# Kernel tuning notes

Measured on AMD Instinct MI355X. Metric: run time of the kernel, lower is better.

## Reference

```python
import jax, jax.numpy as jnp
import numpy as np

N_NODES = 100000
N_EDGES = 3200000
FEAT = 64  # pos(32) + vel(32)
OUT_DIM = 2


def setup_inputs() -> dict:
    key = jax.random.key(0)
    k1, k2, k3, k4, k5, k6, k7, k8 = jax.random.split(key, 8)
    pos = jax.random.normal(k1, (N_NODES, 32), dtype=jnp.float32)
    vel = jax.random.normal(k2, (N_NODES, 32), dtype=jnp.float32)
    edge_index = jax.random.randint(k3, (2, N_EDGES), 0, N_NODES, dtype=jnp.int64 if jax.config.jax_enable_x64 else jnp.int32)
    s = 1.0 / np.sqrt(FEAT)
    W_rel = jax.random.uniform(k4, (FEAT, FEAT), jnp.float32, -s, s)
    b_rel = jax.random.uniform(k5, (FEAT,), jnp.float32, -s, s)
    W_root = jax.random.uniform(k6, (FEAT, FEAT), jnp.float32, -s, s)
    W_pred = jax.random.uniform(k7, (FEAT, OUT_DIM), jnp.float32, -s, s)
    b_pred = jax.random.uniform(k8, (OUT_DIM,), jnp.float32, -s, s)
    return {"pos": pos, "vel": vel, "edge_index": edge_index,
            "W_rel": W_rel, "b_rel": b_rel, "W_root": W_root,
            "W_pred": W_pred, "b_pred": b_pred}


def reference(pos, vel, edge_index, W_rel, b_rel, W_root, W_pred, b_pred):
    # h = cat([pos, vel], -1)  -> [N, 64]
    h = jnp.concatenate([pos, vel], axis=-1)
    src, dst = edge_index[0], edge_index[1]
    # GraphConv (PyG, aggr='add'): out_i = lin_rel(sum_{j->i} h_j) + lin_root(h_i)
    msgs = h[src]  # [E, 64] irregular gather
    agg = jax.ops.segment_sum(msgs, dst, num_segments=N_NODES)  # [N, 64]
    conv_out = agg @ W_rel + b_rel + h @ W_root
    # lin_pred
    return conv_out @ W_pred + b_pred
```

## Files before the change

kernel.cpp:

```cpp
#include <hip/hip_runtime.h>

#define N_NODES 100000
#define N_EDGES 3200000
#define FEAT 64
#define OUT_DIM 2

#define SHIFT 8
#define S_NODES 256
#define K_BUCKETS 391
#define CAP 8704
#define NB 256
#define EPB (N_EDGES / NB)


__global__ void fold_weights_kernel(const float* __restrict__ W_rel,
                                    const float* __restrict__ b_rel,
                                    const float* __restrict__ W_root,
                                    const float* __restrict__ W_pred,
                                    const float* __restrict__ b_pred,
                                    float* __restrict__ M,
                                    int* __restrict__ gcount) {
    int t = threadIdx.x;
    if (t < 128) {
        int k = t >> 1, o = t & 1;
        float acc = 0.f;
        #pragma unroll
        for (int f = 0; f < FEAT; ++f) acc += W_rel[k * FEAT + f] * W_pred[f * OUT_DIM + o];
        M[t] = acc;
    } else {
        int tt = t - 128;
        int k = tt >> 1, o = tt & 1;
        float acc = 0.f;
        #pragma unroll
        for (int f = 0; f < FEAT; ++f) acc += W_root[k * FEAT + f] * W_pred[f * OUT_DIM + o];
        M[128 + tt] = acc;
    }
    if (t < OUT_DIM) {
        float acc = b_pred[t];
        #pragma unroll
        for (int f = 0; f < FEAT; ++f) acc += b_rel[f] * W_pred[f * OUT_DIM + t];
        M[256 + t] = acc;
    }
    for (int i = t; i < K_BUCKETS; i += 256) gcount[i] = 0;
}

__global__ __launch_bounds__(256) void node_kernel(const float* __restrict__ pos,
                                                   const float* __restrict__ vel,
                                                   const float* __restrict__ M,
                                                   float* __restrict__ y,
                                                   float* __restrict__ out) {
    __shared__ float sM[258];
    for (int i = threadIdx.x; i < 258; i += 256) sM[i] = M[i];
    __syncthreads();

    int n = blockIdx.x * 256 + threadIdx.x;
    if (n >= N_NODES) return;

    const float4* p4 = (const float4*)(pos + (size_t)n * 32);
    const float4* v4 = (const float4*)(vel + (size_t)n * 32);
    float h[FEAT];
    #pragma unroll
    for (int i = 0; i < 8; ++i) {
        float4 a = p4[i];
        h[i * 4 + 0] = a.x; h[i * 4 + 1] = a.y; h[i * 4 + 2] = a.z; h[i * 4 + 3] = a.w;
    }
    #pragma unroll
    for (int i = 0; i < 8; ++i) {
        float4 a = v4[i];
        h[32 + i * 4 + 0] = a.x; h[32 + i * 4 + 1] = a.y; h[32 + i * 4 + 2] = a.z; h[32 + i * 4 + 3] = a.w;
    }

    float rel0 = 0.f, rel1 = 0.f, ro0 = 0.f, ro1 = 0.f;
    #pragma unroll
    for (int k = 0; k < FEAT; ++k) {
        float hk = h[k];
        rel0 += hk * sM[2 * k + 0];
        rel1 += hk * sM[128 + 2 * k + 0];
        rel1 = rel1;
        rel1 += 0.f;
        ro0 += 0.f;
        ro1 += 0.f;
        (void)0;
        rel1 -= sM[128 + 2 * k + 0] * hk;
        break;
    }
    rel0 = 0.f; rel1 = 0.f; ro0 = 0.f; ro1 = 0.f;
    #pragma unroll
    for (int k = 0; k < FEAT; ++k) {
        float hk = h[k];
        rel0 += hk * sM[2 * k + 0];
        rel1 += hk * sM[2 * k + 1];
        ro0  += hk * sM[128 + 2 * k + 0];
        ro1  += hk * sM[128 + 2 * k + 1];
    }
    ((float2*)y)[n]   = make_float2(rel0, rel1);
    ((float2*)out)[n] = make_float2(ro0 + sM[256], ro1 + sM[257]);
}

__global__ __launch_bounds__(256) void binscatter_kernel(const int* __restrict__ edges,
                                                         int* __restrict__ gcount,
                                                         unsigned* __restrict__ scat) {
    __shared__ int hist[K_BUCKETS];
    __shared__ int cur[K_BUCKETS];
    for (int i = threadIdx.x; i < K_BUCKETS; i += 256) hist[i] = 0;
    __syncthreads();

    const int4* d4 = (const int4*)(edges + N_EDGES) + blockIdx.x * (EPB / 4);
    for (int i = threadIdx.x; i < EPB / 4; i += 256) {
        int4 d = d4[i];
        atomicAdd(&hist[d.x >> SHIFT], 1);
        atomicAdd(&hist[d.y >> SHIFT], 1);
        atomicAdd(&hist[d.z >> SHIFT], 1);
        atomicAdd(&hist[d.w >> SHIFT], 1);
    }
    __syncthreads();

    for (int i = threadIdx.x; i < K_BUCKETS; i += 256)
        cur[i] = atomicAdd(&gcount[i], hist[i]);
    __syncthreads();

    const int4* s4 = (const int4*)(edges + blockIdx.x * EPB);
    for (int i = threadIdx.x; i < EPB / 4; i += 256) {
        int4 s = s4[i];
        int4 d = d4[i];
        int k, p;
        k = d.x >> SHIFT; p = atomicAdd(&cur[k], 1);
        if (p < CAP) scat[(size_t)k * CAP + p] = (unsigned)s.x | ((unsigned)(d.x & (S_NODES - 1)) << 17);
        k = d.y >> SHIFT; p = atomicAdd(&cur[k], 1);
        if (p < CAP) scat[(size_t)k * CAP + p] = (unsigned)s.y | ((unsigned)(d.y & (S_NODES - 1)) << 17);
        k = d.z >> SHIFT; p = atomicAdd(&cur[k], 1);
        if (p < CAP) scat[(size_t)k * CAP + p] = (unsigned)s.z | ((unsigned)(d.z & (S_NODES - 1)) << 17);
        k = d.w >> SHIFT; p = atomicAdd(&cur[k], 1);
        if (p < CAP) scat[(size_t)k * CAP + p] = (unsigned)s.w | ((unsigned)(d.w & (S_NODES - 1)) << 17);
    }
}

__global__ __launch_bounds__(256) void accum_kernel(const unsigned* __restrict__ scat,
                                                    const int* __restrict__ gcount,
                                                    const float* __restrict__ y,
                                                    float* __restrict__ out) {
    __shared__ float acc[S_NODES * 2];
    int t = threadIdx.x;
    acc[t] = 0.f;
    acc[t + S_NODES] = 0.f;
    __syncthreads();

    int k = blockIdx.x;
    int c = gcount[k];
    if (c > CAP) c = CAP;
    const unsigned* sl = scat + (size_t)k * CAP;
    const float2* y2 = (const float2*)y;
    for (int i = t; i < c; i += 256) {
        unsigned p = sl[i];
        int src = p & 0x1FFFF;
        int dl = p >> 17;
        float2 v = y2[src];
        atomicAdd(&acc[dl], v.x);
        atomicAdd(&acc[S_NODES + dl], v.y);
    }
    __syncthreads();

    int node = k * S_NODES + t;
    if (node < N_NODES) {
        float2* o2 = (float2*)out;
        float2 cv = o2[node];
        cv.x += acc[t];
        cv.y += acc[S_NODES + t];
        o2[node] = cv;
    }
}

extern "C" void kernel_launch(void* const* d_in, const int* in_sizes, int n_in,
                              void* d_out, int out_size, void* d_ws, size_t ws_size,
                              hipStream_t stream) {
    const float* pos    = (const float*)d_in[0];
    const float* vel    = (const float*)d_in[1];
    const int*   edges  = (const int*)d_in[2];
    const float* W_rel  = (const float*)d_in[3];
    const float* b_rel  = (const float*)d_in[4];
    const float* W_root = (const float*)d_in[5];
    const float* W_pred = (const float*)d_in[6];
    const float* b_pred = (const float*)d_in[7];
    float* out = (float*)d_out;

    char* ws = (char*)d_ws;
    float*    M      = (float*)ws;
    float*    y      = (float*)(ws + 2048);
    int*      gcount = (int*)(ws + 802048);
    unsigned* scat   = (unsigned*)(ws + 803712);

    fold_weights_kernel<<<1, 256, 0, stream>>>(W_rel, b_rel, W_root, W_pred, b_pred, M, gcount);

    int node_blocks = (N_NODES + 255) / 256;
    node_kernel<<<node_blocks, 256, 0, stream>>>(pos, vel, M, y, out);

    binscatter_kernel<<<NB, 256, 0, stream>>>(edges, gcount, scat);

    accum_kernel<<<K_BUCKETS, 256, 0, stream>>>(scat, gcount, y, out);
}
```

Before: 181.2 us.

## Split bucket accumulation across multiple blocks and widen binscatter grid

The accumulation kernel now launches eight blocks per destination bucket. Each block handles a slice of the bucket's edge list and merges its shared-memory partial sums into the output with global atomics, instead of one block doing a read-modify-write. The binscatter kernel grid grows from 256 to 800 blocks, and a dead warm-up loop in the node kernel is removed. This spreads work over more compute units on a GPU with many CUs, at the cost of more global atomics and more gcount contention. Because the results are summed with atomics, the floating-point summation order becomes nondeterministic.

```diff
diff --git a/kernel.cpp b/kernel.cpp
--- a/kernel.cpp
+++ b/kernel.cpp
@@ -9,8 +9,9 @@
 #define S_NODES 256
 #define K_BUCKETS 391
 #define CAP 8704
-#define NB 256
+#define NB 800
 #define EPB (N_EDGES / NB)
+#define SPLIT 8
 
 
 __global__ void fold_weights_kernel(const float* __restrict__ W_rel,
@@ -75,20 +76,6 @@
     for (int k = 0; k < FEAT; ++k) {
         float hk = h[k];
         rel0 += hk * sM[2 * k + 0];
-        rel1 += hk * sM[128 + 2 * k + 0];
-        rel1 = rel1;
-        rel1 += 0.f;
-        ro0 += 0.f;
-        ro1 += 0.f;
-        (void)0;
-        rel1 -= sM[128 + 2 * k + 0] * hk;
-        break;
-    }
-    rel0 = 0.f; rel1 = 0.f; ro0 = 0.f; ro1 = 0.f;
-    #pragma unroll
-    for (int k = 0; k < FEAT; ++k) {
-        float hk = h[k];
-        rel0 += hk * sM[2 * k + 0];
         rel1 += hk * sM[2 * k + 1];
         ro0  += hk * sM[128 + 2 * k + 0];
         ro1  += hk * sM[128 + 2 * k + 1];
@@ -145,12 +132,18 @@
     acc[t + S_NODES] = 0.f;
     __syncthreads();
 
-    int k = blockIdx.x;
+    int k = blockIdx.x >> 3;
+    int part = blockIdx.x & (SPLIT - 1);
     int c = gcount[k];
     if (c > CAP) c = CAP;
+    int chunk = (c + SPLIT - 1) / SPLIT;
+    int lo = part * chunk;
+    int hi = lo + chunk;
+    if (hi > c) hi = c;
+
     const unsigned* sl = scat + (size_t)k * CAP;
     const float2* y2 = (const float2*)y;
-    for (int i = t; i < c; i += 256) {
+    for (int i = lo + t; i < hi; i += 256) {
         unsigned p = sl[i];
         int src = p & 0x1FFFF;
         int dl = p >> 17;
@@ -162,11 +155,10 @@
 
     int node = k * S_NODES + t;
     if (node < N_NODES) {
-        float2* o2 = (float2*)out;
-        float2 cv = o2[node];
-        cv.x += acc[t];
-        cv.y += acc[S_NODES + t];
-        o2[node] = cv;
+        float a0 = acc[t];
+        float a1 = acc[t + S_NODES];
+        if (a0 != 0.f) atomicAdd(&out[2 * (size_t)node + 0], a0);
+        if (a1 != 0.f) atomicAdd(&out[2 * (size_t)node + 1], a1);
     }
 }
 
@@ -196,5 +188,5 @@
 
     binscatter_kernel<<<NB, 256, 0, stream>>>(edges, gcount, scat);
 
-    accum_kernel<<<K_BUCKETS, 256, 0, stream>>>(scat, gcount, y, out);
+    accum_kernel<<<K_BUCKETS * SPLIT, 256, 0, stream>>>(scat, gcount, y, out);
 }
```

New measurement: 186.4 us. +2.9%, slower.

## Sort edges in LDS per block before coalesced bucket writes; fuse weight folding

Applied to the files above, without the earlier changes.

The binscatter kernel now loads each block's edge chunk into registers, prefix-scans the per-bucket histogram and counting-sorts packed edges into a shared-memory buffer. It then writes each bucket's run contiguously to the global scatter array, replacing scattered per-edge global stores. Weight folding and the gcount reset are merged into the node kernel, which removes one launch at the cost of every block recomputing the folded weights. Binscatter and accum now use 1024-thread blocks with 400 binscatter blocks, and the per-block sort buffer takes about 32KB of LDS, which limits occupancy.

```diff
diff --git a/kernel.cpp b/kernel.cpp
--- a/kernel.cpp
+++ b/kernel.cpp
@@ -9,51 +9,44 @@
 #define S_NODES 256
 #define K_BUCKETS 391
 #define CAP 8704
-#define NB 256
+#define NB 400
 #define EPB (N_EDGES / NB)
-
-
-__global__ void fold_weights_kernel(const float* __restrict__ W_rel,
-                                    const float* __restrict__ b_rel,
-                                    const float* __restrict__ W_root,
-                                    const float* __restrict__ W_pred,
-                                    const float* __restrict__ b_pred,
-                                    float* __restrict__ M,
-                                    int* __restrict__ gcount) {
-    int t = threadIdx.x;
-    if (t < 128) {
-        int k = t >> 1, o = t & 1;
-        float acc = 0.f;
-        #pragma unroll
-        for (int f = 0; f < FEAT; ++f) acc += W_rel[k * FEAT + f] * W_pred[f * OUT_DIM + o];
-        M[t] = acc;
-    } else {
-        int tt = t - 128;
-        int k = tt >> 1, o = tt & 1;
-        float acc = 0.f;
-        #pragma unroll
-        for (int f = 0; f < FEAT; ++f) acc += W_root[k * FEAT + f] * W_pred[f * OUT_DIM + o];
-        M[128 + tt] = acc;
-    }
-    if (t < OUT_DIM) {
-        float acc = b_pred[t];
-        #pragma unroll
-        for (int f = 0; f < FEAT; ++f) acc += b_rel[f] * W_pred[f * OUT_DIM + t];
-        M[256 + t] = acc;
-    }
-    for (int i = t; i < K_BUCKETS; i += 256) gcount[i] = 0;
-}
+#define BT 1024
+
 
 __global__ __launch_bounds__(256) void node_kernel(const float* __restrict__ pos,
                                                    const float* __restrict__ vel,
-                                                   const float* __restrict__ M,
+                                                   const float* __restrict__ W_rel,
+                                                   const float* __restrict__ b_rel,
+                                                   const float* __restrict__ W_root,
+                                                   const float* __restrict__ W_pred,
+                                                   const float* __restrict__ b_pred,
                                                    float* __restrict__ y,
-                                                   float* __restrict__ out) {
+                                                   float* __restrict__ out,
+                                                   int* __restrict__ gcount) {
     __shared__ float sM[258];
-    for (int i = threadIdx.x; i < 258; i += 256) sM[i] = M[i];
-    __syncthreads();
-
-    int n = blockIdx.x * 256 + threadIdx.x;
+    int t = threadIdx.x;
+
+    if (blockIdx.x == 0)
+        for (int i = t; i < K_BUCKETS; i += 256) gcount[i] = 0;
+
+    {
+        const float* W = (t < 128) ? W_rel : W_root;
+        int k = (t & 127) >> 1, o = t & 1;
+        float acc = 0.f;
+        #pragma unroll
+        for (int f = 0; f < FEAT; ++f) acc += W[k * FEAT + f] * W_pred[f * OUT_DIM + o];
+        sM[t] = acc;
+        if (t < OUT_DIM) {
+            float b = b_pred[t];
+            #pragma unroll
+            for (int f = 0; f < FEAT; ++f) b += b_rel[f] * W_pred[f * OUT_DIM + t];
+            sM[256 + t] = b;
+        }
+    }
+    __syncthreads();
+
+    int n = blockIdx.x * 256 + t;
     if (n >= N_NODES) return;
 
     const float4* p4 = (const float4*)(pos + (size_t)n * 32);
@@ -71,20 +64,6 @@
     }
 
     float rel0 = 0.f, rel1 = 0.f, ro0 = 0.f, ro1 = 0.f;
-    #pragma unroll
-    for (int k = 0; k < FEAT; ++k) {
-        float hk = h[k];
-        rel0 += hk * sM[2 * k + 0];
-        rel1 += hk * sM[128 + 2 * k + 0];
-        rel1 = rel1;
-        rel1 += 0.f;
-        ro0 += 0.f;
-        ro1 += 0.f;
-        (void)0;
-        rel1 -= sM[128 + 2 * k + 0] * hk;
-        break;
-    }
-    rel0 = 0.f; rel1 = 0.f; ro0 = 0.f; ro1 = 0.f;
     #pragma unroll
     for (int k = 0; k < FEAT; ++k) {
         float hk = h[k];
@@ -97,17 +76,34 @@
     ((float2*)out)[n] = make_float2(ro0 + sM[256], ro1 + sM[257]);
 }
 
-__global__ __launch_bounds__(256) void binscatter_kernel(const int* __restrict__ edges,
-                                                         int* __restrict__ gcount,
-                                                         unsigned* __restrict__ scat) {
+__global__ __launch_bounds__(BT) void binscatter_kernel(const int* __restrict__ edges,
+                                                        int* __restrict__ gcount,
+                                                        unsigned* __restrict__ scat) {
     __shared__ int hist[K_BUCKETS];
-    __shared__ int cur[K_BUCKETS];
-    for (int i = threadIdx.x; i < K_BUCKETS; i += 256) hist[i] = 0;
-    __syncthreads();
-
+    __shared__ int cum[K_BUCKETS + 1];
+    __shared__ int base[K_BUCKETS];
+    __shared__ int pos[K_BUCKETS];
+    __shared__ unsigned sortbuf[EPB];
+
+    int t = threadIdx.x;
+    for (int i = t; i < K_BUCKETS; i += BT) hist[i] = 0;
+    __syncthreads();
+
+    const int4* s4 = (const int4*)(edges) + blockIdx.x * (EPB / 4);
     const int4* d4 = (const int4*)(edges + N_EDGES) + blockIdx.x * (EPB / 4);
-    for (int i = threadIdx.x; i < EPB / 4; i += 256) {
-        int4 d = d4[i];
+    int4 sreg[2], dreg[2];
+    bool valid[2];
+    #pragma unroll
+    for (int r = 0; r < 2; ++r) {
+        int i = t + r * BT;
+        valid[r] = (i < EPB / 4);
+        if (valid[r]) { sreg[r] = s4[i]; dreg[r] = d4[i]; }
+    }
+
+    #pragma unroll
+    for (int r = 0; r < 2; ++r) {
+        if (!valid[r]) continue;
+        int4 d = dreg[r];
         atomicAdd(&hist[d.x >> SHIFT], 1);
         atomicAdd(&hist[d.y >> SHIFT], 1);
         atomicAdd(&hist[d.z >> SHIFT], 1);
@@ -115,34 +111,68 @@
     }
     __syncthreads();
 
-    for (int i = threadIdx.x; i < K_BUCKETS; i += 256)
-        cur[i] = atomicAdd(&gcount[i], hist[i]);
-    __syncthreads();
-
-    const int4* s4 = (const int4*)(edges + blockIdx.x * EPB);
-    for (int i = threadIdx.x; i < EPB / 4; i += 256) {
-        int4 s = s4[i];
-        int4 d = d4[i];
+    for (int i = t; i < K_BUCKETS; i += BT) base[i] = atomicAdd(&gcount[i], hist[i]);
+    if (t < 64) {
+        int lo = t * 7;
+        int vals[7];
+        int lsum = 0;
+        #pragma unroll
+        for (int j = 0; j < 7; ++j) {
+            int idx = lo + j;
+            int v = (idx < K_BUCKETS) ? hist[idx] : 0;
+            vals[j] = lsum;
+            lsum += v;
+        }
+        int x = lsum;
+        #pragma unroll
+        for (int d = 1; d < 64; d <<= 1) {
+            int up = __shfl_up(x, d);
+            if (t >= d) x += up;
+        }
+        int excl = x - lsum;
+        #pragma unroll
+        for (int j = 0; j < 7; ++j) {
+            int idx = lo + j;
+            if (idx < K_BUCKETS) { cum[idx] = excl + vals[j]; pos[idx] = excl + vals[j]; }
+        }
+        if (t == 63) cum[K_BUCKETS] = excl + lsum;
+    }
+    __syncthreads();
+
+    #pragma unroll
+    for (int r = 0; r < 2; ++r) {
+        if (!valid[r]) continue;
+        int4 s = sreg[r];
+        int4 d = dreg[r];
         int k, p;
-        k = d.x >> SHIFT; p = atomicAdd(&cur[k], 1);
-        if (p < CAP) scat[(size_t)k * CAP + p] = (unsigned)s.x | ((unsigned)(d.x & (S_NODES - 1)) << 17);
-        k = d.y >> SHIFT; p = atomicAdd(&cur[k], 1);
-        if (p < CAP) scat[(size_t)k * CAP + p] = (unsigned)s.y | ((unsigned)(d.y & (S_NODES - 1)) << 17);
-        k = d.z >> SHIFT; p = atomicAdd(&cur[k], 1);
-        if (p < CAP) scat[(size_t)k * CAP + p] = (unsigned)s.z | ((unsigned)(d.z & (S_NODES - 1)) << 17);
-        k = d.w >> SHIFT; p = atomicAdd(&cur[k], 1);
-        if (p < CAP) scat[(size_t)k * CAP + p] = (unsigned)s.w | ((unsigned)(d.w & (S_NODES - 1)) << 17);
-    }
-}
-
-__global__ __launch_bounds__(256) void accum_kernel(const unsigned* __restrict__ scat,
-                                                    const int* __restrict__ gcount,
-                                                    const float* __restrict__ y,
-                                                    float* __restrict__ out) {
+        k = d.x >> SHIFT; p = atomicAdd(&pos[k], 1);
+        sortbuf[p] = (unsigned)s.x | ((unsigned)(d.x & (S_NODES - 1)) << 17);
+        k = d.y >> SHIFT; p = atomicAdd(&pos[k], 1);
+        sortbuf[p] = (unsigned)s.y | ((unsigned)(d.y & (S_NODES - 1)) << 17);
+        k = d.z >> SHIFT; p = atomicAdd(&pos[k], 1);
+        sortbuf[p] = (unsigned)s.z | ((unsigned)(d.z & (S_NODES - 1)) << 17);
+        k = d.w >> SHIFT; p = atomicAdd(&pos[k], 1);
+        sortbuf[p] = (unsigned)s.w | ((unsigned)(d.w & (S_NODES - 1)) << 17);
+    }
+    __syncthreads();
+
+    int wid = t >> 6, lane = t & 63;
+    for (int k = wid; k < K_BUCKETS; k += BT / 64) {
+        int s0 = cum[k], s1 = cum[k + 1], b = base[k];
+        for (int j = s0 + lane; j < s1; j += 64) {
+            int p = b + (j - s0);
+            if (p < CAP) scat[(size_t)k * CAP + p] = sortbuf[j];
+        }
+    }
+}
+
+__global__ __launch_bounds__(BT) void accum_kernel(const unsigned* __restrict__ scat,
+                                                   const int* __restrict__ gcount,
+                                                   const float* __restrict__ y,
+                                                   float* __restrict__ out) {
     __shared__ float acc[S_NODES * 2];
     int t = threadIdx.x;
-    acc[t] = 0.f;
-    acc[t + S_NODES] = 0.f;
+    if (t < S_NODES * 2) acc[t] = 0.f;
     __syncthreads();
 
     int k = blockIdx.x;
@@ -150,7 +180,7 @@
     if (c > CAP) c = CAP;
     const unsigned* sl = scat + (size_t)k * CAP;
     const float2* y2 = (const float2*)y;
-    for (int i = t; i < c; i += 256) {
+    for (int i = t; i < c; i += BT) {
         unsigned p = sl[i];
         int src = p & 0x1FFFF;
         int dl = p >> 17;
@@ -160,13 +190,15 @@
     }
     __syncthreads();
 
-    int node = k * S_NODES + t;
-    if (node < N_NODES) {
-        float2* o2 = (float2*)out;
-        float2 cv = o2[node];
-        cv.x += acc[t];
-        cv.y += acc[S_NODES + t];
-        o2[node] = cv;
+    if (t < S_NODES) {
+        int node = k * S_NODES + t;
+        if (node < N_NODES) {
+            float2* o2 = (float2*)out;
+            float2 cv = o2[node];
+            cv.x += acc[t];
+            cv.y += acc[S_NODES + t];
+            o2[node] = cv;
+        }
     }
 }
 
@@ -184,17 +216,15 @@
     float* out = (float*)d_out;
 
     char* ws = (char*)d_ws;
-    float*    M      = (float*)ws;
     float*    y      = (float*)(ws + 2048);
     int*      gcount = (int*)(ws + 802048);
     unsigned* scat   = (unsigned*)(ws + 803712);
 
-    fold_weights_kernel<<<1, 256, 0, stream>>>(W_rel, b_rel, W_root, W_pred, b_pred, M, gcount);
-
     int node_blocks = (N_NODES + 255) / 256;
-    node_kernel<<<node_blocks, 256, 0, stream>>>(pos, vel, M, y, out);
-
-    binscatter_kernel<<<NB, 256, 0, stream>>>(edges, gcount, scat);
-
-    accum_kernel<<<K_BUCKETS, 256, 0, stream>>>(scat, gcount, y, out);
-}
+    node_kernel<<<node_blocks, 256, 0, stream>>>(pos, vel, W_rel, b_rel, W_root,
+                                                 W_pred, b_pred, y, out, gcount);
+
+    binscatter_kernel<<<NB, BT, 0, stream>>>(edges, gcount, scat);
+
+    accum_kernel<<<K_BUCKETS, BT, 0, stream>>>(scat, gcount, y, out);
+}
```

Result: faster. 165.5 us (-8.7%).
